# Kernel optimization log

Measured on AMD Instinct MI355X. Metric: run time of the kernel, lower is better.

## Reference

```python
import jax, jax.numpy as jnp
import numpy as np

N_NODES = 100000
N_EDGES = 1600000
IN_FEATS = 128
HID = 128      # 2 * n_hidden
OUT = 64       # n_hidden


def setup_inputs() -> dict:
    key = jax.random.key(0)
    ks = jax.random.split(key, 10)
    features = jax.random.normal(ks[0], (N_NODES, IN_FEATS), dtype=jnp.float32)
    src = jax.random.randint(ks[1], (N_EDGES,), 0, N_NODES)
    dst = jax.random.randint(ks[2], (N_EDGES,), 0, N_NODES)
    s0 = 1.0 / np.sqrt(IN_FEATS)
    s1 = 1.0 / np.sqrt(HID)
    W_self0 = jax.random.uniform(ks[3], (IN_FEATS, HID), minval=-s0, maxval=s0, dtype=jnp.float32)
    W_neigh0 = jax.random.uniform(ks[4], (IN_FEATS, HID), minval=-s0, maxval=s0, dtype=jnp.float32)
    b0 = jnp.zeros((HID,), dtype=jnp.float32)
    W_self1 = jax.random.uniform(ks[5], (HID, OUT), minval=-s1, maxval=s1, dtype=jnp.float32)
    W_neigh1 = jax.random.uniform(ks[6], (HID, OUT), minval=-s1, maxval=s1, dtype=jnp.float32)
    b1 = jnp.zeros((OUT,), dtype=jnp.float32)
    return {"features": features, "src": src, "dst": dst,
            "W_self0": W_self0, "W_neigh0": W_neigh0, "b0": b0,
            "W_self1": W_self1, "W_neigh1": W_neigh1, "b1": b1}


def _mean_agg(x, src, dst, n_nodes):
    # gather neighbor feats along edges, sum per destination, divide by in-degree
    summed = jax.ops.segment_sum(x[src], dst, num_segments=n_nodes)  # [N, d]
    deg = jax.ops.segment_sum(jnp.ones((src.shape[0],), x.dtype), dst, num_segments=n_nodes)
    deg = jnp.maximum(deg, 1.0)[:, None]
    return summed / deg


def _sage_layer(x, src, dst, W_self, W_neigh, b, act):
    agg = _mean_agg(x, src, dst, x.shape[0])
    out = x @ W_self + agg @ W_neigh + b
    return jax.nn.relu(out) if act else out


def reference(features, src, dst, W_self0, W_neigh0, b0, W_self1, W_neigh1, b1):
    h = _sage_layer(features, src, dst, W_self0, W_neigh0, b0, act=True)
    h = _sage_layer(h, src, dst, W_self1, W_neigh1, b1, act=False)
    return h
```

## Files before the change

kernel.cpp:

```cpp
#include <hip/hip_runtime.h>

#define N_NODES 100000
#define N_EDGES 1600000
#define CAP 60
#define OVF_CAP 8192
#define GBLK 782
#define NBIN 1563
#define BINCAP2 1280
#define FBLK 12500
#define ZROW 100000

typedef unsigned int uint;
typedef unsigned short ushort;
typedef __attribute__((ext_vector_type(8))) short short8;
typedef __attribute__((ext_vector_type(4))) float f32x4;

__device__ __forceinline__ ushort f2bf(float f) {
  uint x = __float_as_uint(f);
  x += 0x7fffu + ((x >> 16) & 1u);
  return (ushort)(x >> 16);
}
__device__ __forceinline__ float bflo(uint u) {
  return __uint_as_float(u << 16);
}
__device__ __forceinline__ float bfhi(uint u) {
  return __uint_as_float(u & 0xffff0000u);
}
__device__ __forceinline__ f32x4 uplo(uint4 u) {
  return (f32x4){bflo(u.x), bfhi(u.x), bflo(u.y), bfhi(u.y)};
}
__device__ __forceinline__ f32x4 uphi(uint4 u) {
  return (f32x4){bflo(u.z), bfhi(u.z), bflo(u.w), bfhi(u.w)};
}

__global__ __launch_bounds__(256) void k_pb(
    const int* __restrict__ src, const int* __restrict__ dst,
    const float* __restrict__ feat, const float* __restrict__ Ws0,
    const float* __restrict__ Wn0, const float* __restrict__ Ws1,
    const float* __restrict__ Wn1, uint* __restrict__ gcursor,
    uint* __restrict__ binbuf, int* __restrict__ ovf_cnt,
    int* __restrict__ ovf, uint* __restrict__ fbfu, ushort* __restrict__ wp0,
    ushort* __restrict__ wp1) {
  __shared__ uint hist[NBIN];
  __shared__ uint base[NBIN];
  int b = blockIdx.x;
  int tid = threadIdx.x;
  if (b < GBLK) {
    for (int i = tid; i < NBIN; i += 256) hist[i] = 0;
    __syncthreads();
    int e0 = b * 2048;
    uint val[8], bn[8], rk[8];
    int vld[8];
#pragma unroll
    for (int it = 0; it < 8; ++it) {
      int e = e0 + it * 256 + tid;
      vld[it] = (e < N_EDGES);
      if (vld[it]) {
        uint s = (uint)src[e];
        uint d = (uint)dst[e];
        bn[it] = d >> 6;
        rk[it] = atomicAdd(&hist[bn[it]], 1u);
        val[it] = s | ((d & 63u) << 17);
      }
    }
    __syncthreads();
    for (int i = tid; i < NBIN; i += 256)
      base[i] = hist[i] ? atomicAdd(&gcursor[i], hist[i]) : 0u;
    __syncthreads();
#pragma unroll
    for (int it = 0; it < 8; ++it) {
      if (!vld[it]) continue;
      uint p = base[bn[it]] + rk[it];
      if (p < BINCAP2) {
        binbuf[(size_t)bn[it] * BINCAP2 + p] = val[it];
      } else {
        int o = atomicAdd(ovf_cnt, 1);
        if (o < OVF_CAP) {
          ovf[2 * o] = (int)(val[it] & 0x1FFFFu);
          ovf[2 * o + 1] = (int)(bn[it] * 64 + (val[it] >> 17));
        }
      }
    }
    return;
  }
  if (b < GBLK + FBLK) {
    int i = (b - GBLK) * 256 + tid;
    float4 v = reinterpret_cast<const float4*>(feat)[i];
    uint2 o;
    o.x = (uint)f2bf(v.x) | ((uint)f2bf(v.y) << 16);
    o.y = (uint)f2bf(v.z) | ((uint)f2bf(v.w) << 16);
    reinterpret_cast<uint2*>(fbfu)[i] = o;
    return;
  }
  int wb = b - GBLK - FBLK;
  if (wb >= 192) {
    if (tid < 64) fbfu[ZROW * 64 + tid] = 0;
    return;
  }
  int idx = wb * 256 + tid;
  if (idx < 32768) {
    int k = idx >> 7, n = idx & 127;
    float v = (k < 128) ? Ws0[k * 128 + n] : Wn0[(k - 128) * 128 + n];
    int s = k >> 5, q = (k >> 3) & 3, j = k & 7;
    int t = n >> 4, c = n & 15;
    wp0[(((s * 8 + t) * 64) + (q * 16 + c)) * 8 + j] = f2bf(v);
  } else {
    int i2 = idx - 32768;
    int k = i2 >> 7, n = i2 & 127;
    float v = (n < 64) ? Wn1[k * 64 + n] : Ws1[k * 64 + (n - 64)];
    int s = k >> 5, q = (k >> 3) & 3, j = k & 7;
    int t = n >> 4, c = n & 15;
    wp1[(((s * 8 + t) * 64) + (q * 16 + c)) * 8 + j] = f2bf(v);
  }
}

__global__ __launch_bounds__(256) void k_agg0(
    const uint4* __restrict__ fbf4, const uint* __restrict__ binbuf,
    const uint* __restrict__ gcursor, int* __restrict__ ovf_cnt,
    int* __restrict__ ovf, uint4* __restrict__ agg4) {
  __shared__ __attribute__((aligned(16))) int lbkt[64 * CAP];
  __shared__ uint lcnt[64];
  int bb = blockIdx.x;
  int tid = threadIdx.x;
  if (tid < 64) lcnt[tid] = 0;
#pragma unroll
  for (int i = tid; i < 64 * CAP; i += 256) lbkt[i] = ZROW;
  __syncthreads();
  int ne = min((int)gcursor[bb], BINCAP2);
  for (int i = tid; i < ne; i += 256) {
    uint v = binbuf[(size_t)bb * BINCAP2 + i];
    int ldl = (int)(v >> 17);
    uint pos = atomicAdd(&lcnt[ldl], 1u);
    if (pos < CAP) {
      lbkt[ldl * CAP + pos] = (int)(v & 0x1FFFFu);
    } else {
      int o = atomicAdd(ovf_cnt, 1);
      if (o < OVF_CAP) {
        ovf[2 * o] = (int)(v & 0x1FFFFu);
        ovf[2 * o + 1] = (bb * 64 + ldl) | (1 << 30);
      }
    }
  }
  __syncthreads();
  int g = tid >> 4, li = tid & 15;
  const int4* lb4 = reinterpret_cast<const int4*>(lbkt);
  int oc = min(*ovf_cnt, OVF_CAP);
#pragma unroll
  for (int p = 0; p < 4; ++p) {
    int nl = p * 16 + g;
    int n = bb * 64 + nl;
    int c = (int)lcnt[nl];
    int kb = min(c, CAP);
    f32x4 accA = (f32x4){0.f, 0.f, 0.f, 0.f};
    f32x4 accB = (f32x4){0.f, 0.f, 0.f, 0.f};
    for (int j = 0; j < kb; j += 12) {
      int4 ia = lb4[nl * 15 + (j >> 2)];
      int4 ib = lb4[nl * 15 + (j >> 2) + 1];
      int4 ic = lb4[nl * 15 + (j >> 2) + 2];
      uint4 u0 = fbf4[(size_t)ia.x * 16 + li];
      uint4 u1 = fbf4[(size_t)ia.y * 16 + li];
      uint4 u2 = fbf4[(size_t)ia.z * 16 + li];
      uint4 u3 = fbf4[(size_t)ia.w * 16 + li];
      uint4 u4 = fbf4[(size_t)ib.x * 16 + li];
      uint4 u5 = fbf4[(size_t)ib.y * 16 + li];
      uint4 u6 = fbf4[(size_t)ib.z * 16 + li];
      uint4 u7 = fbf4[(size_t)ib.w * 16 + li];
      uint4 u8 = fbf4[(size_t)ic.x * 16 + li];
      uint4 u9 = fbf4[(size_t)ic.y * 16 + li];
      uint4 ua = fbf4[(size_t)ic.z * 16 + li];
      uint4 ub = fbf4[(size_t)ic.w * 16 + li];
      accA += uplo(u0); accB += uphi(u0);
      accA += uplo(u1); accB += uphi(u1);
      accA += uplo(u2); accB += uphi(u2);
      accA += uplo(u3); accB += uphi(u3);
      accA += uplo(u4); accB += uphi(u4);
      accA += uplo(u5); accB += uphi(u5);
      accA += uplo(u6); accB += uphi(u6);
      accA += uplo(u7); accB += uphi(u7);
      accA += uplo(u8); accB += uphi(u8);
      accA += uplo(u9); accB += uphi(u9);
      accA += uplo(ua); accB += uphi(ua);
      accA += uplo(ub); accB += uphi(ub);
    }
    for (int i = 0; i < oc; ++i) {
      int df = ovf[2 * i + 1];
      if ((df & 0x1FFFF) == n) {
        uint4 u = fbf4[(size_t)ovf[2 * i] * 16 + li];
        accA += uplo(u);
        accB += uphi(u);
        c += ((df >> 30) & 1) ^ 1;
      }
    }
    float inv = 1.f / (float)max(c, 1);
    accA *= inv;
    accB *= inv;
    if (n < N_NODES) {
      uint4 o;
      o.x = (uint)f2bf(accA.x) | ((uint)f2bf(accA.y) << 16);
      o.y = (uint)f2bf(accA.z) | ((uint)f2bf(accA.w) << 16);
      o.z = (uint)f2bf(accB.x) | ((uint)f2bf(accB.y) << 16);
      o.w = (uint)f2bf(accB.z) | ((uint)f2bf(accB.w) << 16);
      agg4[(size_t)n * 16 + li] = o;
    }
  }
}

__global__ __launch_bounds__(256) void k_gemm0(
    const ushort* __restrict__ fbf, const ushort* aggb,
    const uint4* __restrict__ wp0g, const float* __restrict__ b0,
    ushort* h) {
  __shared__ uint4 wlds[4096];
  int tid = threadIdx.x;
#pragma unroll
  for (int i = 0; i < 16; ++i) wlds[i * 256 + tid] = wp0g[i * 256 + tid];
  __syncthreads();
  const short8* wl8 = reinterpret_cast<const short8*>(wlds);

  int lane = tid & 63, w = tid >> 6;
  int quad = lane >> 4, lm = lane & 15;
  int mw = blockIdx.x * 128 + (w >> 1) * 64;
  int tgb = (w & 1) * 4;

  f32x4 acc[4][4];
#pragma unroll
  for (int rt = 0; rt < 4; ++rt)
#pragma unroll
    for (int ct = 0; ct < 4; ++ct) acc[rt][ct] = (f32x4){0.f, 0.f, 0.f, 0.f};
  short8 az = {0, 0, 0, 0, 0, 0, 0, 0};

#pragma unroll
  for (int s = 0; s < 8; ++s) {
    const ushort* bsrc = (s < 4) ? fbf : aggb;
    int koff = (s & 3) * 32 + quad * 8;
    short8 a[4];
#pragma unroll
    for (int rt = 0; rt < 4; ++rt) {
      int row = mw + rt * 16 + lm;
      a[rt] = (row < N_NODES)
                  ? *reinterpret_cast<const short8*>(bsrc + (size_t)row * 128 + koff)
                  : az;
    }
#pragma unroll
    for (int ct = 0; ct < 4; ++ct) {
      short8 b = wl8[(s * 8 + tgb + ct) * 64 + lane];
#pragma unroll
      for (int rt = 0; rt < 4; ++rt)
        acc[rt][ct] =
            __builtin_amdgcn_mfma_f32_16x16x32_bf16(a[rt], b, acc[rt][ct], 0, 0, 0);
    }
  }

  __syncthreads();
  float bv[4];
#pragma unroll
  for (int ct = 0; ct < 4; ++ct) bv[ct] = b0[(tgb + ct) * 16 + lm];
#pragma unroll
  for (int rt = 0; rt < 4; ++rt)
#pragma unroll
    for (int ct = 0; ct < 4; ++ct)
#pragma unroll
      for (int i = 0; i < 4; ++i) {
        int row = mw + rt * 16 + quad * 4 + i;
        if (row < N_NODES) {
          int col = (tgb + ct) * 16 + lm;
          h[(size_t)row * 128 + col] = f2bf(fmaxf(acc[rt][ct][i] + bv[ct], 0.f));
        }
      }
}

__global__ __launch_bounds__(256) void k_gemm1(
    const ushort* __restrict__ h, const uint4* __restrict__ wp1g,
    const float* __restrict__ b1, ushort* __restrict__ hw,
    float* __restrict__ out) {
  __shared__ uint4 wlds[2048];
  int tid = threadIdx.x;
  if (blockIdx.x == 0 && tid < 8)
    reinterpret_cast<uint4*>(hw)[ZROW * 8 + tid] = make_uint4(0, 0, 0, 0);
#pragma unroll
  for (int i = 0; i < 8; ++i) wlds[i * 256 + tid] = wp1g[i * 256 + tid];
  __syncthreads();
  const short8* wl8 = reinterpret_cast<const short8*>(wlds);

  int lane = tid & 63, w = tid >> 6;
  int quad = lane >> 4, lm = lane & 15;
  int mw = blockIdx.x * 128 + (w >> 1) * 64;
  int tgb = (w & 1) * 4;

  f32x4 acc[4][4];
#pragma unroll
  for (int rt = 0; rt < 4; ++rt)
#pragma unroll
    for (int ct = 0; ct < 4; ++ct) acc[rt][ct] = (f32x4){0.f, 0.f, 0.f, 0.f};
  short8 az = {0, 0, 0, 0, 0, 0, 0, 0};

#pragma unroll
  for (int s = 0; s < 4; ++s) {
    int koff = s * 32 + quad * 8;
    short8 a[4];
#pragma unroll
    for (int rt = 0; rt < 4; ++rt) {
      int row = mw + rt * 16 + lm;
      a[rt] = (row < N_NODES)
                  ? *reinterpret_cast<const short8*>(h + (size_t)row * 128 + koff)
                  : az;
    }
#pragma unroll
    for (int ct = 0; ct < 4; ++ct) {
      short8 b = wl8[(s * 8 + tgb + ct) * 64 + lane];
#pragma unroll
      for (int rt = 0; rt < 4; ++rt)
        acc[rt][ct] =
            __builtin_amdgcn_mfma_f32_16x16x32_bf16(a[rt], b, acc[rt][ct], 0, 0, 0);
    }
  }

  if ((w & 1) == 0) {
#pragma unroll
    for (int rt = 0; rt < 4; ++rt)
#pragma unroll
      for (int ct = 0; ct < 4; ++ct)
#pragma unroll
        for (int i = 0; i < 4; ++i) {
          int row = mw + rt * 16 + quad * 4 + i;
          if (row < N_NODES)
            hw[(size_t)row * 64 + ct * 16 + lm] = f2bf(acc[rt][ct][i]);
        }
  } else {
    float bv[4];
#pragma unroll
    for (int ct = 0; ct < 4; ++ct) bv[ct] = b1[ct * 16 + lm];
#pragma unroll
    for (int rt = 0; rt < 4; ++rt)
#pragma unroll
      for (int ct = 0; ct < 4; ++ct)
#pragma unroll
        for (int i = 0; i < 4; ++i) {
          int row = mw + rt * 16 + quad * 4 + i;
          if (row < N_NODES)
            out[(size_t)row * 64 + ct * 16 + lm] = acc[rt][ct][i] + bv[ct];
        }
  }
}

__global__ __launch_bounds__(256) void k_agg1(
    const uint4* __restrict__ hw4, const uint* __restrict__ binbuf,
    const uint* __restrict__ gcursor, int* __restrict__ ovf_cnt,
    int* __restrict__ ovf, float* __restrict__ out) {
  __shared__ __attribute__((aligned(16))) int lbkt[64 * CAP];
  __shared__ uint lcnt[64];
  int bb = blockIdx.x;
  int tid = threadIdx.x;
  if (tid < 64) lcnt[tid] = 0;
#pragma unroll
  for (int i = tid; i < 64 * CAP; i += 256) lbkt[i] = ZROW;
  __syncthreads();
  int ne = min((int)gcursor[bb], BINCAP2);
  for (int i = tid; i < ne; i += 256) {
    uint v = binbuf[(size_t)bb * BINCAP2 + i];
    int ldl = (int)(v >> 17);
    uint pos = atomicAdd(&lcnt[ldl], 1u);
    if (pos < CAP) lbkt[ldl * CAP + pos] = (int)(v & 0x1FFFFu);
  }
  __syncthreads();
  int g = tid >> 3, li = tid & 7;
  const int4* lb4 = reinterpret_cast<const int4*>(lbkt);
  int oc = min(*ovf_cnt, OVF_CAP);
#pragma unroll
  for (int p = 0; p < 2; ++p) {
    int nl = p * 32 + g;
    int n = bb * 64 + nl;
    int c = (int)lcnt[nl];
    int kb = min(c, CAP);
    f32x4 accA = (f32x4){0.f, 0.f, 0.f, 0.f};
    f32x4 accB = (f32x4){0.f, 0.f, 0.f, 0.f};
    for (int j = 0; j < kb; j += 12) {
      int4 ia = lb4[nl * 15 + (j >> 2)];
      int4 ib = lb4[nl * 15 + (j >> 2) + 1];
      int4 ic = lb4[nl * 15 + (j >> 2) + 2];
      uint4 u0 = hw4[(size_t)ia.x * 8 + li];
      uint4 u1 = hw4[(size_t)ia.y * 8 + li];
      uint4 u2 = hw4[(size_t)ia.z * 8 + li];
      uint4 u3 = hw4[(size_t)ia.w * 8 + li];
      uint4 u4 = hw4[(size_t)ib.x * 8 + li];
      uint4 u5 = hw4[(size_t)ib.y * 8 + li];
      uint4 u6 = hw4[(size_t)ib.z * 8 + li];
      uint4 u7 = hw4[(size_t)ib.w * 8 + li];
      uint4 u8 = hw4[(size_t)ic.x * 8 + li];
      uint4 u9 = hw4[(size_t)ic.y * 8 + li];
      uint4 ua = hw4[(size_t)ic.z * 8 + li];
      uint4 ub = hw4[(size_t)ic.w * 8 + li];
      accA += uplo(u0); accB += uphi(u0);
      accA += uplo(u1); accB += uphi(u1);
      accA += uplo(u2); accB += uphi(u2);
      accA += uplo(u3); accB += uphi(u3);
      accA += uplo(u4); accB += uphi(u4);
      accA += uplo(u5); accB += uphi(u5);
      accA += uplo(u6); accB += uphi(u6);
      accA += uplo(u7); accB += uphi(u7);
      accA += uplo(u8); accB += uphi(u8);
      accA += uplo(u9); accB += uphi(u9);
      accA += uplo(ua); accB += uphi(ua);
      accA += uplo(ub); accB += uphi(ub);
    }
    for (int i = 0; i < oc; ++i) {
      int df = ovf[2 * i + 1];
      if ((df & 0x1FFFF) == n) {
        uint4 u = hw4[(size_t)ovf[2 * i] * 8 + li];
        accA += uplo(u);
        accB += uphi(u);
        c += ((df >> 30) & 1) ^ 1;
      }
    }
    if (n < N_NODES) {
      float inv = 1.f / (float)max(c, 1);
      float* op = out + (size_t)n * 64 + li * 8;
      float4 c0 = *reinterpret_cast<float4*>(op);
      float4 c1 = *reinterpret_cast<float4*>(op + 4);
      c0.x += accA.x * inv;
      c0.y += accA.y * inv;
      c0.z += accA.z * inv;
      c0.w += accA.w * inv;
      c1.x += accB.x * inv;
      c1.y += accB.y * inv;
      c1.z += accB.z * inv;
      c1.w += accB.w * inv;
      *reinterpret_cast<float4*>(op) = c0;
      *reinterpret_cast<float4*>(op + 4) = c1;
    }
  }
}

extern "C" void kernel_launch(void* const* d_in, const int* in_sizes, int n_in,
                              void* d_out, int out_size, void* d_ws,
                              size_t ws_size, hipStream_t stream) {
  const float* feat = (const float*)d_in[0];
  const int* src = (const int*)d_in[1];
  const int* dst = (const int*)d_in[2];
  const float* Ws0 = (const float*)d_in[3];
  const float* Wn0 = (const float*)d_in[4];
  const float* b0 = (const float*)d_in[5];
  const float* Ws1 = (const float*)d_in[6];
  const float* Wn1 = (const float*)d_in[7];
  const float* b1 = (const float*)d_in[8];
  char* ws = (char*)d_ws;

  ushort* hbuf = (ushort*)(ws);
  int* ovf_cnt = (int*)(ws + 25600000);
  uint* gcursor = (uint*)(ws + 25600064);
  int* ovf = (int*)(ws + 25606400);
  uint* binbuf = (uint*)(ws + 25671936);
  ushort* fbf = (ushort*)(ws + 33674496);
  ushort* hw = (ushort*)(ws + 33674496);
  ushort* wp0 = (ushort*)(ws + 59274752);
  ushort* wp1 = (ushort*)(ws + 59340288);
  float* out = (float*)d_out;

  hipMemsetAsync(ws + 25600000, 0, 6400, stream);
  k_pb<<<GBLK + FBLK + 193, 256, 0, stream>>>(src, dst, feat, Ws0, Wn0, Ws1,
                                              Wn1, gcursor, binbuf, ovf_cnt,
                                              ovf, (uint*)fbf, wp0, wp1);
  k_agg0<<<NBIN, 256, 0, stream>>>((const uint4*)fbf, binbuf, gcursor, ovf_cnt,
                                   ovf, (uint4*)hbuf);
  k_gemm0<<<GBLK, 256, 0, stream>>>(fbf, hbuf, (const uint4*)wp0, b0, hbuf);
  k_gemm1<<<GBLK, 256, 0, stream>>>(hbuf, (const uint4*)wp1, b1, hw, out);
  k_agg1<<<NBIN, 256, 0, stream>>>((const uint4*)hw, binbuf, gcursor, ovf_cnt,
                                   ovf, out);
}
```

Baseline: 288.1 us.

## Pipeline neighbor gathers via async global-to-LDS loads and pad bin cursors

Both aggregation kernels now issue neighbor-row gathers with global_load_lds into a per-wave LDS ring of depth 4. Each wave walks its node groups as one flat stream, using a wave-wide max neighbor count and explicit vmcnt waits to keep several loads in flight. The old 12-way unrolled register gather is removed. The global bin cursors are spaced 64 bytes apart to reduce atomic contention, and the workspace offsets and memset grow to match. The cost is extra dummy loads for lanes whose node has fewer neighbors than the wave max, plus hand-written waitcnt logic that is fragile.

```diff
diff --git a/kernel.cpp b/kernel.cpp
--- a/kernel.cpp
+++ b/kernel.cpp
@@ -9,6 +9,7 @@
 #define BINCAP2 1280
 #define FBLK 12500
 #define ZROW 100000
+#define DEPTH 4
 
 typedef unsigned int uint;
 typedef unsigned short ushort;
@@ -31,6 +32,23 @@
 }
 __device__ __forceinline__ f32x4 uphi(uint4 u) {
   return (f32x4){bflo(u.z), bfhi(u.z), bflo(u.w), bfhi(u.w)};
+}
+
+__device__ __forceinline__ void gl_lds16(const uint4* g, uint4* l) {
+  __builtin_amdgcn_global_load_lds(
+      (const __attribute__((address_space(1))) uint*)g,
+      (__attribute__((address_space(3))) uint*)l, 16, 0, 0);
+}
+__device__ __forceinline__ int wmax16(int v) {
+  v = max(v, __shfl_xor(v, 16));
+  v = max(v, __shfl_xor(v, 32));
+  return v;
+}
+__device__ __forceinline__ int wmax8(int v) {
+  v = max(v, __shfl_xor(v, 8));
+  v = max(v, __shfl_xor(v, 16));
+  v = max(v, __shfl_xor(v, 32));
+  return v;
 }
 
 __global__ __launch_bounds__(256) void k_pb(
@@ -42,7 +60,6 @@
     int* __restrict__ ovf, uint* __restrict__ fbfu, ushort* __restrict__ wp0,
     ushort* __restrict__ wp1) {
   __shared__ uint hist[NBIN];
-  __shared__ uint base[NBIN];
   int b = blockIdx.x;
   int tid = threadIdx.x;
   if (b < GBLK) {
@@ -64,13 +81,15 @@
       }
     }
     __syncthreads();
-    for (int i = tid; i < NBIN; i += 256)
-      base[i] = hist[i] ? atomicAdd(&gcursor[i], hist[i]) : 0u;
+    for (int i = tid; i < NBIN; i += 256) {
+      uint h = hist[i];
+      hist[i] = h ? atomicAdd(&gcursor[i * 16], h) : 0u;
+    }
     __syncthreads();
 #pragma unroll
     for (int it = 0; it < 8; ++it) {
       if (!vld[it]) continue;
-      uint p = base[bn[it]] + rk[it];
+      uint p = hist[bn[it]] + rk[it];
       if (p < BINCAP2) {
         binbuf[(size_t)bn[it] * BINCAP2 + p] = val[it];
       } else {
@@ -120,13 +139,13 @@
     int* __restrict__ ovf, uint4* __restrict__ agg4) {
   __shared__ __attribute__((aligned(16))) int lbkt[64 * CAP];
   __shared__ uint lcnt[64];
+  __shared__ __attribute__((aligned(16))) uint4 gbuf[4 * DEPTH * 64];
   int bb = blockIdx.x;
   int tid = threadIdx.x;
   if (tid < 64) lcnt[tid] = 0;
-#pragma unroll
   for (int i = tid; i < 64 * CAP; i += 256) lbkt[i] = ZROW;
   __syncthreads();
-  int ne = min((int)gcursor[bb], BINCAP2);
+  int ne = min((int)gcursor[bb * 16], BINCAP2);
   for (int i = tid; i < ne; i += 256) {
     uint v = binbuf[(size_t)bb * BINCAP2 + i];
     int ldl = (int)(v >> 17);
@@ -142,46 +161,27 @@
     }
   }
   __syncthreads();
-  int g = tid >> 4, li = tid & 15;
-  const int4* lb4 = reinterpret_cast<const int4*>(lbkt);
+
+  int w = tid >> 6, lane = tid & 63;
+  int sub = lane >> 4, li = lane & 15;
+  uint4* slab = &gbuf[w * (DEPTH * 64)];
   int oc = min(*ovf_cnt, OVF_CAP);
-#pragma unroll
-  for (int p = 0; p < 4; ++p) {
-    int nl = p * 16 + g;
+
+  int kb0 = min((int)lcnt[w * 16 + sub], CAP);
+  int kb1 = min((int)lcnt[w * 16 + 4 + sub], CAP);
+  int kb2 = min((int)lcnt[w * 16 + 8 + sub], CAP);
+  int kb3 = min((int)lcnt[w * 16 + 12 + sub], CAP);
+  int mg0 = wmax16(kb0), mg1 = wmax16(kb1), mg2 = wmax16(kb2),
+      mg3 = wmax16(kb3);
+  int T = mg0 + mg1 + mg2 + mg3;
+  auto MG = [&](int g) { return g == 0 ? mg0 : g == 1 ? mg1 : g == 2 ? mg2 : mg3; };
+
+  f32x4 accA = (f32x4){0.f, 0.f, 0.f, 0.f};
+  f32x4 accB = (f32x4){0.f, 0.f, 0.f, 0.f};
+  auto FIN = [&](int g) {
+    int nl = w * 16 + g * 4 + sub;
     int n = bb * 64 + nl;
     int c = (int)lcnt[nl];
-    int kb = min(c, CAP);
-    f32x4 accA = (f32x4){0.f, 0.f, 0.f, 0.f};
-    f32x4 accB = (f32x4){0.f, 0.f, 0.f, 0.f};
-    for (int j = 0; j < kb; j += 12) {
-      int4 ia = lb4[nl * 15 + (j >> 2)];
-      int4 ib = lb4[nl * 15 + (j >> 2) + 1];
-      int4 ic = lb4[nl * 15 + (j >> 2) + 2];
-      uint4 u0 = fbf4[(size_t)ia.x * 16 + li];
-      uint4 u1 = fbf4[(size_t)ia.y * 16 + li];
-      uint4 u2 = fbf4[(size_t)ia.z * 16 + li];
-      uint4 u3 = fbf4[(size_t)ia.w * 16 + li];
-      uint4 u4 = fbf4[(size_t)ib.x * 16 + li];
-      uint4 u5 = fbf4[(size_t)ib.y * 16 + li];
-      uint4 u6 = fbf4[(size_t)ib.z * 16 + li];
-      uint4 u7 = fbf4[(size_t)ib.w * 16 + li];
-      uint4 u8 = fbf4[(size_t)ic.x * 16 + li];
-      uint4 u9 = fbf4[(size_t)ic.y * 16 + li];
-      uint4 ua = fbf4[(size_t)ic.z * 16 + li];
-      uint4 ub = fbf4[(size_t)ic.w * 16 + li];
-      accA += uplo(u0); accB += uphi(u0);
-      accA += uplo(u1); accB += uphi(u1);
-      accA += uplo(u2); accB += uphi(u2);
-      accA += uplo(u3); accB += uphi(u3);
-      accA += uplo(u4); accB += uphi(u4);
-      accA += uplo(u5); accB += uphi(u5);
-      accA += uplo(u6); accB += uphi(u6);
-      accA += uplo(u7); accB += uphi(u7);
-      accA += uplo(u8); accB += uphi(u8);
-      accA += uplo(u9); accB += uphi(u9);
-      accA += uplo(ua); accB += uphi(ua);
-      accA += uplo(ub); accB += uphi(ub);
-    }
     for (int i = 0; i < oc; ++i) {
       int df = ovf[2 * i + 1];
       if ((df & 0x1FFFF) == n) {
@@ -191,18 +191,52 @@
         c += ((df >> 30) & 1) ^ 1;
       }
     }
-    float inv = 1.f / (float)max(c, 1);
-    accA *= inv;
-    accB *= inv;
     if (n < N_NODES) {
+      float inv = 1.f / (float)max(c, 1);
+      f32x4 rA = accA * inv, rB = accB * inv;
       uint4 o;
-      o.x = (uint)f2bf(accA.x) | ((uint)f2bf(accA.y) << 16);
-      o.y = (uint)f2bf(accA.z) | ((uint)f2bf(accA.w) << 16);
-      o.z = (uint)f2bf(accB.x) | ((uint)f2bf(accB.y) << 16);
-      o.w = (uint)f2bf(accB.z) | ((uint)f2bf(accB.w) << 16);
+      o.x = (uint)f2bf(rA.x) | ((uint)f2bf(rA.y) << 16);
+      o.y = (uint)f2bf(rA.z) | ((uint)f2bf(rA.w) << 16);
+      o.z = (uint)f2bf(rB.x) | ((uint)f2bf(rB.y) << 16);
+      o.w = (uint)f2bf(rB.z) | ((uint)f2bf(rB.w) << 16);
       agg4[(size_t)n * 16 + li] = o;
     }
-  }
+    accA = (f32x4){0.f, 0.f, 0.f, 0.f};
+    accB = (f32x4){0.f, 0.f, 0.f, 0.f};
+  };
+  auto ISSUE = [&](int gi, int ji, int slot) {
+    int s = ZROW;
+    if (gi < 4) s = lbkt[(w * 16 + gi * 4 + sub) * CAP + ji];
+    gl_lds16(fbf4 + (size_t)s * 16 + li, slab + slot * 64);
+  };
+
+  int gi = 0, ji = 0;
+  while (gi < 4 && MG(gi) == 0) gi++;
+  for (int k = 0; k < DEPTH; ++k) {
+    ISSUE(gi, ji, k);
+    if (gi < 4) {
+      ji++;
+      while (gi < 4 && ji >= MG(gi)) { gi++; ji = 0; }
+    }
+  }
+  int gc = 0, jc = 0;
+  while (gc < 4 && MG(gc) == 0) { FIN(gc); gc++; }
+  for (int t = 0; t < T; ++t) {
+    asm volatile("s_waitcnt vmcnt(3)" ::: "memory");
+    __builtin_amdgcn_sched_barrier(0);
+    uint4 u = slab[(t & (DEPTH - 1)) * 64 + lane];
+    accA += uplo(u);
+    accB += uphi(u);
+    __builtin_amdgcn_sched_barrier(0);
+    ISSUE(gi, ji, t & (DEPTH - 1));
+    if (gi < 4) {
+      ji++;
+      while (gi < 4 && ji >= MG(gi)) { gi++; ji = 0; }
+    }
+    jc++;
+    while (gc < 4 && jc >= MG(gc)) { FIN(gc); gc++; jc = 0; }
+  }
+  asm volatile("s_waitcnt vmcnt(0)" ::: "memory");
 }
 
 __global__ __launch_bounds__(256) void k_gemm0(
@@ -348,13 +382,13 @@
     int* __restrict__ ovf, float* __restrict__ out) {
   __shared__ __attribute__((aligned(16))) int lbkt[64 * CAP];
   __shared__ uint lcnt[64];
+  __shared__ __attribute__((aligned(16))) uint4 gbuf[4 * DEPTH * 64];
   int bb = blockIdx.x;
   int tid = threadIdx.x;
   if (tid < 64) lcnt[tid] = 0;
-#pragma unroll
   for (int i = tid; i < 64 * CAP; i += 256) lbkt[i] = ZROW;
   __syncthreads();
-  int ne = min((int)gcursor[bb], BINCAP2);
+  int ne = min((int)gcursor[bb * 16], BINCAP2);
   for (int i = tid; i < ne; i += 256) {
     uint v = binbuf[(size_t)bb * BINCAP2 + i];
     int ldl = (int)(v >> 17);
@@ -362,46 +396,24 @@
     if (pos < CAP) lbkt[ldl * CAP + pos] = (int)(v & 0x1FFFFu);
   }
   __syncthreads();
-  int g = tid >> 3, li = tid & 7;
-  const int4* lb4 = reinterpret_cast<const int4*>(lbkt);
+
+  int w = tid >> 6, lane = tid & 63;
+  int sub = lane >> 3, li = lane & 7;
+  uint4* slab = &gbuf[w * (DEPTH * 64)];
   int oc = min(*ovf_cnt, OVF_CAP);
-#pragma unroll
-  for (int p = 0; p < 2; ++p) {
-    int nl = p * 32 + g;
+
+  int kb0 = min((int)lcnt[w * 16 + sub], CAP);
+  int kb1 = min((int)lcnt[w * 16 + 8 + sub], CAP);
+  int mg0 = wmax8(kb0), mg1 = wmax8(kb1);
+  int T = mg0 + mg1;
+  auto MG = [&](int g) { return g == 0 ? mg0 : mg1; };
+
+  f32x4 accA = (f32x4){0.f, 0.f, 0.f, 0.f};
+  f32x4 accB = (f32x4){0.f, 0.f, 0.f, 0.f};
+  auto FIN = [&](int g) {
+    int nl = w * 16 + g * 8 + sub;
     int n = bb * 64 + nl;
     int c = (int)lcnt[nl];
-    int kb = min(c, CAP);
-    f32x4 accA = (f32x4){0.f, 0.f, 0.f, 0.f};
-    f32x4 accB = (f32x4){0.f, 0.f, 0.f, 0.f};
-    for (int j = 0; j < kb; j += 12) {
-      int4 ia = lb4[nl * 15 + (j >> 2)];
-      int4 ib = lb4[nl * 15 + (j >> 2) + 1];
-      int4 ic = lb4[nl * 15 + (j >> 2) + 2];
-      uint4 u0 = hw4[(size_t)ia.x * 8 + li];
-      uint4 u1 = hw4[(size_t)ia.y * 8 + li];
-      uint4 u2 = hw4[(size_t)ia.z * 8 + li];
-      uint4 u3 = hw4[(size_t)ia.w * 8 + li];
-      uint4 u4 = hw4[(size_t)ib.x * 8 + li];
-      uint4 u5 = hw4[(size_t)ib.y * 8 + li];
-      uint4 u6 = hw4[(size_t)ib.z * 8 + li];
-      uint4 u7 = hw4[(size_t)ib.w * 8 + li];
-      uint4 u8 = hw4[(size_t)ic.x * 8 + li];
-      uint4 u9 = hw4[(size_t)ic.y * 8 + li];
-      uint4 ua = hw4[(size_t)ic.z * 8 + li];
-      uint4 ub = hw4[(size_t)ic.w * 8 + li];
-      accA += uplo(u0); accB += uphi(u0);
-      accA += uplo(u1); accB += uphi(u1);
-      accA += uplo(u2); accB += uphi(u2);
-      accA += uplo(u3); accB += uphi(u3);
-      accA += uplo(u4); accB += uphi(u4);
-      accA += uplo(u5); accB += uphi(u5);
-      accA += uplo(u6); accB += uphi(u6);
-      accA += uplo(u7); accB += uphi(u7);
-      accA += uplo(u8); accB += uphi(u8);
-      accA += uplo(u9); accB += uphi(u9);
-      accA += uplo(ua); accB += uphi(ua);
-      accA += uplo(ub); accB += uphi(ub);
-    }
     for (int i = 0; i < oc; ++i) {
       int df = ovf[2 * i + 1];
       if ((df & 0x1FFFF) == n) {
@@ -427,7 +439,42 @@
       *reinterpret_cast<float4*>(op) = c0;
       *reinterpret_cast<float4*>(op + 4) = c1;
     }
-  }
+    accA = (f32x4){0.f, 0.f, 0.f, 0.f};
+    accB = (f32x4){0.f, 0.f, 0.f, 0.f};
+  };
+  auto ISSUE = [&](int gi, int ji, int slot) {
+    int s = ZROW;
+    if (gi < 2) s = lbkt[(w * 16 + gi * 8 + sub) * CAP + ji];
+    gl_lds16(hw4 + (size_t)s * 8 + li, slab + slot * 64);
+  };
+
+  int gi = 0, ji = 0;
+  while (gi < 2 && MG(gi) == 0) gi++;
+  for (int k = 0; k < DEPTH; ++k) {
+    ISSUE(gi, ji, k);
+    if (gi < 2) {
+      ji++;
+      while (gi < 2 && ji >= MG(gi)) { gi++; ji = 0; }
+    }
+  }
+  int gc = 0, jc = 0;
+  while (gc < 2 && MG(gc) == 0) { FIN(gc); gc++; }
+  for (int t = 0; t < T; ++t) {
+    asm volatile("s_waitcnt vmcnt(3)" ::: "memory");
+    __builtin_amdgcn_sched_barrier(0);
+    uint4 u = slab[(t & (DEPTH - 1)) * 64 + lane];
+    accA += uplo(u);
+    accB += uphi(u);
+    __builtin_amdgcn_sched_barrier(0);
+    ISSUE(gi, ji, t & (DEPTH - 1));
+    if (gi < 2) {
+      ji++;
+      while (gi < 2 && ji >= MG(gi)) { gi++; ji = 0; }
+    }
+    jc++;
+    while (gc < 2 && jc >= MG(gc)) { FIN(gc); gc++; jc = 0; }
+  }
+  asm volatile("s_waitcnt vmcnt(0)" ::: "memory");
 }
 
 extern "C" void kernel_launch(void* const* d_in, const int* in_sizes, int n_in,
@@ -447,15 +494,15 @@
   ushort* hbuf = (ushort*)(ws);
   int* ovf_cnt = (int*)(ws + 25600000);
   uint* gcursor = (uint*)(ws + 25600064);
-  int* ovf = (int*)(ws + 25606400);
-  uint* binbuf = (uint*)(ws + 25671936);
-  ushort* fbf = (ushort*)(ws + 33674496);
-  ushort* hw = (ushort*)(ws + 33674496);
-  ushort* wp0 = (ushort*)(ws + 59274752);
-  ushort* wp1 = (ushort*)(ws + 59340288);
+  int* ovf = (int*)(ws + 25700096);
+  uint* binbuf = (uint*)(ws + 25765632);
+  ushort* fbf = (ushort*)(ws + 33768192);
+  ushort* hw = (ushort*)(ws + 33768192);
+  ushort* wp0 = (ushort*)(ws + 59368448);
+  ushort* wp1 = (ushort*)(ws + 59433984);
   float* out = (float*)d_out;
 
-  hipMemsetAsync(ws + 25600000, 0, 6400, stream);
+  hipMemsetAsync(ws + 25600000, 0, 100096, stream);
   k_pb<<<GBLK + FBLK + 193, 256, 0, stream>>>(src, dst, feat, Ws0, Wn0, Ws1,
                                               Wn1, gcursor, binbuf, ovf_cnt,
                                               ovf, (uint*)fbf, wp0, wp1);
```

Measured after the change: 362.6 us. 1.26x slower.

## Fuse layer-0 and layer-1 GEMMs through an LDS-resident hidden tile

Applied to the files above, without the earlier changes.

The two GEMM kernels merge into one. The layer-0 output tile (bias plus ReLU, in bf16) is written into a 128x128 XOR-swizzled LDS tile and fed straight into the layer-1 MFMA, so the hidden activations no longer round-trip through global memory and one launch is removed. Weights are now read from global or L2 directly instead of being staged in LDS. The global bin cursors are padded to 16-element stride to avoid atomic contention on shared cache lines. The workspace layout is moved so that hw no longer aliases fbf, and hw's zero row is set in k_pb.

```diff
diff --git a/kernel.cpp b/kernel.cpp
--- a/kernel.cpp
+++ b/kernel.cpp
@@ -39,10 +39,9 @@
     const float* __restrict__ Wn0, const float* __restrict__ Ws1,
     const float* __restrict__ Wn1, uint* __restrict__ gcursor,
     uint* __restrict__ binbuf, int* __restrict__ ovf_cnt,
-    int* __restrict__ ovf, uint* __restrict__ fbfu, ushort* __restrict__ wp0,
-    ushort* __restrict__ wp1) {
+    int* __restrict__ ovf, uint* __restrict__ fbfu, uint* __restrict__ hwu,
+    ushort* __restrict__ wp0, ushort* __restrict__ wp1) {
   __shared__ uint hist[NBIN];
-  __shared__ uint base[NBIN];
   int b = blockIdx.x;
   int tid = threadIdx.x;
   if (b < GBLK) {
@@ -64,13 +63,15 @@
       }
     }
     __syncthreads();
-    for (int i = tid; i < NBIN; i += 256)
-      base[i] = hist[i] ? atomicAdd(&gcursor[i], hist[i]) : 0u;
+    for (int i = tid; i < NBIN; i += 256) {
+      uint h = hist[i];
+      hist[i] = h ? atomicAdd(&gcursor[i * 16], h) : 0u;
+    }
     __syncthreads();
 #pragma unroll
     for (int it = 0; it < 8; ++it) {
       if (!vld[it]) continue;
-      uint p = base[bn[it]] + rk[it];
+      uint p = hist[bn[it]] + rk[it];
       if (p < BINCAP2) {
         binbuf[(size_t)bn[it] * BINCAP2 + p] = val[it];
       } else {
@@ -95,6 +96,7 @@
   int wb = b - GBLK - FBLK;
   if (wb >= 192) {
     if (tid < 64) fbfu[ZROW * 64 + tid] = 0;
+    else if (tid < 96) hwu[ZROW * 32 + (tid - 64)] = 0;
     return;
   }
   int idx = wb * 256 + tid;
@@ -126,7 +128,7 @@
 #pragma unroll
   for (int i = tid; i < 64 * CAP; i += 256) lbkt[i] = ZROW;
   __syncthreads();
-  int ne = min((int)gcursor[bb], BINCAP2);
+  int ne = min((int)gcursor[bb * 16], BINCAP2);
   for (int i = tid; i < ne; i += 256) {
     uint v = binbuf[(size_t)bb * BINCAP2 + i];
     int ldl = (int)(v >> 17);
@@ -205,20 +207,17 @@
   }
 }
 
-__global__ __launch_bounds__(256) void k_gemm0(
-    const ushort* __restrict__ fbf, const ushort* aggb,
-    const uint4* __restrict__ wp0g, const float* __restrict__ b0,
-    ushort* h) {
-  __shared__ uint4 wlds[4096];
+__global__ __launch_bounds__(256) void k_gemm(
+    const ushort* __restrict__ fbf, const ushort* __restrict__ aggb,
+    const short8* __restrict__ wp0f, const short8* __restrict__ wp1f,
+    const float* __restrict__ b0, const float* __restrict__ b1,
+    ushort* __restrict__ hw, float* __restrict__ out) {
+  __shared__ ushort htile[128 * 128];
   int tid = threadIdx.x;
-#pragma unroll
-  for (int i = 0; i < 16; ++i) wlds[i * 256 + tid] = wp0g[i * 256 + tid];
-  __syncthreads();
-  const short8* wl8 = reinterpret_cast<const short8*>(wlds);
-
   int lane = tid & 63, w = tid >> 6;
   int quad = lane >> 4, lm = lane & 15;
-  int mw = blockIdx.x * 128 + (w >> 1) * 64;
+  int rl0 = (w >> 1) * 64;
+  int mw = blockIdx.x * 128 + rl0;
   int tgb = (w & 1) * 4;
 
   f32x4 acc[4][4];
@@ -242,7 +241,7 @@
     }
 #pragma unroll
     for (int ct = 0; ct < 4; ++ct) {
-      short8 b = wl8[(s * 8 + tgb + ct) * 64 + lane];
+      short8 b = wp0f[(s * 8 + tgb + ct) * 64 + lane];
 #pragma unroll
       for (int rt = 0; rt < 4; ++rt)
         acc[rt][ct] =
@@ -250,48 +249,30 @@
     }
   }
 
+  {
+    float bv[4];
+#pragma unroll
+    for (int ct = 0; ct < 4; ++ct) bv[ct] = b0[(tgb + ct) * 16 + lm];
+#pragma unroll
+    for (int rt = 0; rt < 4; ++rt)
+#pragma unroll
+      for (int ct = 0; ct < 4; ++ct)
+#pragma unroll
+        for (int i = 0; i < 4; ++i) {
+          int r = rl0 + rt * 16 + quad * 4 + i;
+          float v = (blockIdx.x * 128 + r < N_NODES)
+                        ? fmaxf(acc[rt][ct][i] + bv[ct], 0.f)
+                        : 0.f;
+          int col = (tgb + ct) * 16 + lm;
+          htile[r * 128 + (col ^ ((r & 15) * 8))] = f2bf(v);
+        }
+  }
   __syncthreads();
-  float bv[4];
-#pragma unroll
-  for (int ct = 0; ct < 4; ++ct) bv[ct] = b0[(tgb + ct) * 16 + lm];
+
 #pragma unroll
   for (int rt = 0; rt < 4; ++rt)
 #pragma unroll
-    for (int ct = 0; ct < 4; ++ct)
-#pragma unroll
-      for (int i = 0; i < 4; ++i) {
-        int row = mw + rt * 16 + quad * 4 + i;
-        if (row < N_NODES) {
-          int col = (tgb + ct) * 16 + lm;
-          h[(size_t)row * 128 + col] = f2bf(fmaxf(acc[rt][ct][i] + bv[ct], 0.f));
-        }
-      }
-}
-
-__global__ __launch_bounds__(256) void k_gemm1(
-    const ushort* __restrict__ h, const uint4* __restrict__ wp1g,
-    const float* __restrict__ b1, ushort* __restrict__ hw,
-    float* __restrict__ out) {
-  __shared__ uint4 wlds[2048];
-  int tid = threadIdx.x;
-  if (blockIdx.x == 0 && tid < 8)
-    reinterpret_cast<uint4*>(hw)[ZROW * 8 + tid] = make_uint4(0, 0, 0, 0);
-#pragma unroll
-  for (int i = 0; i < 8; ++i) wlds[i * 256 + tid] = wp1g[i * 256 + tid];
-  __syncthreads();
-  const short8* wl8 = reinterpret_cast<const short8*>(wlds);
-
-  int lane = tid & 63, w = tid >> 6;
-  int quad = lane >> 4, lm = lane & 15;
-  int mw = blockIdx.x * 128 + (w >> 1) * 64;
-  int tgb = (w & 1) * 4;
-
-  f32x4 acc[4][4];
-#pragma unroll
-  for (int rt = 0; rt < 4; ++rt)
-#pragma unroll
     for (int ct = 0; ct < 4; ++ct) acc[rt][ct] = (f32x4){0.f, 0.f, 0.f, 0.f};
-  short8 az = {0, 0, 0, 0, 0, 0, 0, 0};
 
 #pragma unroll
   for (int s = 0; s < 4; ++s) {
@@ -299,14 +280,13 @@
     short8 a[4];
 #pragma unroll
     for (int rt = 0; rt < 4; ++rt) {
-      int row = mw + rt * 16 + lm;
-      a[rt] = (row < N_NODES)
-                  ? *reinterpret_cast<const short8*>(h + (size_t)row * 128 + koff)
-                  : az;
+      int r = rl0 + rt * 16 + lm;
+      a[rt] = *reinterpret_cast<const short8*>(
+          &htile[r * 128 + (koff ^ ((r & 15) * 8))]);
     }
 #pragma unroll
     for (int ct = 0; ct < 4; ++ct) {
-      short8 b = wl8[(s * 8 + tgb + ct) * 64 + lane];
+      short8 b = wp1f[(s * 8 + tgb + ct) * 64 + lane];
 #pragma unroll
       for (int rt = 0; rt < 4; ++rt)
         acc[rt][ct] =
@@ -354,7 +334,7 @@
 #pragma unroll
   for (int i = tid; i < 64 * CAP; i += 256) lbkt[i] = ZROW;
   __syncthreads();
-  int ne = min((int)gcursor[bb], BINCAP2);
+  int ne = min((int)gcursor[bb * 16], BINCAP2);
   for (int i = tid; i < ne; i += 256) {
     uint v = binbuf[(size_t)bb * BINCAP2 + i];
     int ldl = (int)(v >> 17);
@@ -447,22 +427,22 @@
   ushort* hbuf = (ushort*)(ws);
   int* ovf_cnt = (int*)(ws + 25600000);
   uint* gcursor = (uint*)(ws + 25600064);
-  int* ovf = (int*)(ws + 25606400);
-  uint* binbuf = (uint*)(ws + 25671936);
-  ushort* fbf = (ushort*)(ws + 33674496);
-  ushort* hw = (ushort*)(ws + 33674496);
-  ushort* wp0 = (ushort*)(ws + 59274752);
-  ushort* wp1 = (ushort*)(ws + 59340288);
+  int* ovf = (int*)(ws + 25700096);
+  uint* binbuf = (uint*)(ws + 25765632);
+  ushort* fbf = (ushort*)(ws + 33768192);
+  ushort* hw = (ushort*)(ws + 59368448);
+  ushort* wp0 = (ushort*)(ws + 72168576);
+  ushort* wp1 = (ushort*)(ws + 72234112);
   float* out = (float*)d_out;
 
-  hipMemsetAsync(ws + 25600000, 0, 6400, stream);
-  k_pb<<<GBLK + FBLK + 193, 256, 0, stream>>>(src, dst, feat, Ws0, Wn0, Ws1,
-                                              Wn1, gcursor, binbuf, ovf_cnt,
-                                              ovf, (uint*)fbf, wp0, wp1);
+  hipMemsetAsync(ws + 25600000, 0, 100096, stream);
+  k_pb<<<GBLK + FBLK + 193, 256, 0, stream>>>(
+      src, dst, feat, Ws0, Wn0, Ws1, Wn1, gcursor, binbuf, ovf_cnt, ovf,
+      (uint*)fbf, (uint*)hw, wp0, wp1);
   k_agg0<<<NBIN, 256, 0, stream>>>((const uint4*)fbf, binbuf, gcursor, ovf_cnt,
                                    ovf, (uint4*)hbuf);
-  k_gemm0<<<GBLK, 256, 0, stream>>>(fbf, hbuf, (const uint4*)wp0, b0, hbuf);
-  k_gemm1<<<GBLK, 256, 0, stream>>>(hbuf, (const uint4*)wp1, b1, hw, out);
+  k_gemm<<<GBLK, 256, 0, stream>>>(fbf, hbuf, (const short8*)wp0,
+                                   (const short8*)wp1, b0, b1, hw, out);
   k_agg1<<<NBIN, 256, 0, stream>>>((const uint4*)hw, binbuf, gcursor, ovf_cnt,
                                    ovf, out);
 }
```

Result: slower. 301.1 us (+4.5%).
